# Optimization experiments

Hardware: AMD Instinct MI355X
Metric: run time of the kernel (lower is better)

Reference implementation:

```python
import jax, jax.numpy as jnp
import numpy as np

NUM_EMBEDDINGS = 512
EMBEDDING_DIM = 64
COMMITMENT_COST = 0.25


def setup_inputs() -> dict:
    key = jax.random.key(0)
    k1, k2 = jax.random.split(key)
    x = jax.random.normal(k1, (64, 64, 32, 32), dtype=jnp.float32)  # NCHW, C == embedding_dim
    lim = 1.0 / NUM_EMBEDDINGS
    emb = jax.random.uniform(k2, (NUM_EMBEDDINGS, EMBEDDING_DIM), dtype=jnp.float32,
                             minval=-lim, maxval=lim)
    return {"x": x, "emb": emb}


def reference(x, emb):
    # NCHW -> NHWC
    xp = jnp.transpose(x, (0, 2, 3, 1))  # [B,H,W,D]
    B, H, W, D = xp.shape
    flat = xp.reshape(-1, D)  # [N,D]
    dists = (jnp.sum(flat * flat, axis=1, keepdims=True)
             + jnp.sum(emb * emb, axis=1)
             - 2.0 * jnp.matmul(flat, emb.T))
    idx = jnp.argmin(dists, axis=1)  # [N]
    quantized = emb[idx].reshape(B, H, W, D)
    # losses (note: names follow the original module)
    q_latent_loss = jnp.mean((jax.lax.stop_gradient(quantized) - xp) ** 2)
    e_latent_loss = jnp.mean((quantized - jax.lax.stop_gradient(xp)) ** 2)
    loss = e_latent_loss + COMMITMENT_COST * q_latent_loss
    # straight-through estimator
    quantized = xp + jax.lax.stop_gradient(quantized - xp)
    quantized = jnp.transpose(quantized, (0, 3, 1, 2))  # back to NCHW
    return quantized, loss, idx[:, None]
```

## Files before the change

### kernel.cpp

```cpp
#include <hip/hip_runtime.h>
#include <float.h>

#pragma clang fp contract(off)

#define K_EMB   512
#define D_EMB   64
#define Q_ELEMS 4194304
#define NBLK    1024
#define W_SCR   0.5f
#define XROW    65
#define LCAP    1024

typedef _Float16 f16x8 __attribute__((ext_vector_type(8)));
typedef float    f32x4 __attribute__((ext_vector_type(4)));

__device__ __forceinline__ float np_sumsq64(const float* v) {
    float r[8];
    #pragma unroll
    for (int j = 0; j < 8; ++j) r[j] = v[j] * v[j];
    #pragma unroll
    for (int i = 8; i < 64; i += 8) {
        #pragma unroll
        for (int j = 0; j < 8; ++j) {
            float s = v[i + j] * v[i + j];
            r[j] = r[j] + s;
        }
    }
    return ((r[0] + r[1]) + (r[2] + r[3])) + ((r[4] + r[5]) + (r[6] + r[7]));
}

__global__ __launch_bounds__(256) void vq_prep(const float* __restrict__ emb,
                                               float* __restrict__ t2,
                                               float* __restrict__ t2s512,
                                               f16x8* __restrict__ embA) {
    const int g = blockIdx.x * 256 + threadIdx.x;
    if (g < K_EMB) {
        const float* ep = emb + (g << 6);
        float s = np_sumsq64(ep);
        t2[g]     = s;
        t2s512[g] = 512.0f * s;
    }
    if (g < 4096) {
        const int t = g >> 7;
        const int s = (g >> 6) & 1;
        const int l = g & 63;
        const int code  = t * 16 + (l & 15);
        const int dbase = s * 32 + ((l >> 4) << 3);
        const float* ep = emb + (code << 6) + dbase;
        f16x8 a;
        #pragma unroll
        for (int i = 0; i < 8; ++i) a[i] = (_Float16)(512.0f * ep[i]);
        embA[g] = a;
    }
}

__global__ __launch_bounds__(256) void vq_main(const float* __restrict__ x,
                                               const float* __restrict__ emb,
                                               const float* __restrict__ t2,
                                               const float* __restrict__ t2s512,
                                               const f16x8* __restrict__ embA,
                                               float* __restrict__ out_q,
                                               float* __restrict__ out_idx,
                                               float* __restrict__ partial) {
    const int tid  = threadIdx.x;
    const int lane = tid & 63;
    const int wave = tid >> 6;

    __shared__ float xf[64 * XROW];
    __shared__ float t1s[64];
    __shared__ unsigned long long keys[64];
    __shared__ int   list[LCAP];
    __shared__ int   lcnt;
    __shared__ float red[4];

    {
        const int p = tid & 63;
        const int q = tid >> 6;
        const int np_ = blockIdx.x * 64 + p;
        const float* __restrict__ xs = x + (np_ >> 10) * 65536 + (np_ & 1023);
        #pragma unroll
        for (int j = 0; j < 16; ++j) {
            const int d = q * 16 + j;
            xf[p * XROW + d] = xs[d * 1024];
        }
        if (tid < 64) keys[tid] = 0xFFFFFFFFFFFFFFFFull;
        if (tid == 0) lcnt = 0;
    }
    __syncthreads();

    if (wave == 0) t1s[lane] = np_sumsq64(&xf[lane * XROW]);

    const int bp = 16 * wave + (lane & 15);
    const int bg = lane >> 4;
    f16x8 b0, b1;
    #pragma unroll
    for (int i = 0; i < 8; ++i) {
        b0[i] = (_Float16)xf[bp * XROW + 0 * 32 + bg * 8 + i];
        b1[i] = (_Float16)xf[bp * XROW + 1 * 32 + bg * 8 + i];
    }

    const f32x4 czero = {0.f, 0.f, 0.f, 0.f};
    const float4* __restrict__ t2s4 = (const float4*)t2s512;

    float m = FLT_MAX;
    for (int t = 0; t < 32; ++t) {
        f16x8 a0 = embA[(t * 2 + 0) * 64 + lane];
        f16x8 a1 = embA[(t * 2 + 1) * 64 + lane];
        f32x4 c = __builtin_amdgcn_mfma_f32_16x16x32_f16(a0, b0, czero, 0, 0, 0);
        c = __builtin_amdgcn_mfma_f32_16x16x32_f16(a1, b1, c, 0, 0, 0);
        float4 tv = t2s4[t * 4 + bg];
        float s0 = fmaf(-2.f, c[0], tv.x);
        float s1 = fmaf(-2.f, c[1], tv.y);
        float s2 = fmaf(-2.f, c[2], tv.z);
        float s3 = fmaf(-2.f, c[3], tv.w);
        m = fminf(m, fminf(fminf(s0, s1), fminf(s2, s3)));
    }
    m = fminf(m, __shfl_xor(m, 16));
    m = fminf(m, __shfl_xor(m, 32));
    const float thr = m + W_SCR;

    for (int t = 0; t < 32; ++t) {
        f16x8 a0 = embA[(t * 2 + 0) * 64 + lane];
        f16x8 a1 = embA[(t * 2 + 1) * 64 + lane];
        f32x4 c = __builtin_amdgcn_mfma_f32_16x16x32_f16(a0, b0, czero, 0, 0, 0);
        c = __builtin_amdgcn_mfma_f32_16x16x32_f16(a1, b1, c, 0, 0, 0);
        float4 tv = t2s4[t * 4 + bg];
        #pragma unroll
        for (int j = 0; j < 4; ++j) {
            float sj = fmaf(-2.f, c[j], (j == 0) ? tv.x : (j == 1) ? tv.y
                                       : (j == 2) ? tv.z : tv.w);
            if (sj < thr) {
                const int k = t * 16 + bg * 4 + j;
                int slot = atomicAdd(&lcnt, 1);
                if (slot < LCAP) list[slot] = bp * 512 + k;
            }
        }
    }
    __syncthreads();

    const int ncand = min(lcnt, LCAP);
    for (int i = tid; i < ncand; i += 256) {
        const int v = list[i];
        const int p = v >> 9;
        const int k = v & 511;
        const float* xp = &xf[p * XROW];
        const float* __restrict__ ep = emb + (k << 6);
        float a = 0.f;
        #pragma unroll
        for (int d = 0; d < D_EMB; ++d) a = fmaf(xp[d], ep[d], a);
        float X = t1s[p] + t2[k];
        float dnp = fmaf(-2.f, a, X);
        unsigned long long key =
            ((unsigned long long)__float_as_uint(dnp) << 32) | (unsigned)k;
        atomicMin(&keys[p], key);
    }
    __syncthreads();

    float acc = 0.f;
    {
        const int p = tid & 63;
        const int q = tid >> 6;
        const int n2 = blockIdx.x * 64 + p;
        const int kw = (int)(unsigned)(keys[p] & 0xFFFFFFFFull);
        float* __restrict__ qp = out_q + (n2 >> 10) * 65536 + (n2 & 1023);
        const float4* __restrict__ eq = (const float4*)(emb + (kw << 6) + q * 16);
        #pragma unroll
        for (int j4 = 0; j4 < 4; ++j4) {
            float4 qv = eq[j4];
            const int d = q * 16 + j4 * 4;
            float f0 = qv.x - xf[p * XROW + d + 0];
            float f1 = qv.y - xf[p * XROW + d + 1];
            float f2 = qv.z - xf[p * XROW + d + 2];
            float f3 = qv.w - xf[p * XROW + d + 3];
            acc = fmaf(f0, f0, acc);
            acc = fmaf(f1, f1, acc);
            acc = fmaf(f2, f2, acc);
            acc = fmaf(f3, f3, acc);
            qp[(d + 0) * 1024] = qv.x;
            qp[(d + 1) * 1024] = qv.y;
            qp[(d + 2) * 1024] = qv.z;
            qp[(d + 3) * 1024] = qv.w;
        }
        if (q == 0) out_idx[n2] = (float)kw;
    }

    #pragma unroll
    for (int off = 32; off > 0; off >>= 1) acc += __shfl_down(acc, off);
    if (lane == 0) red[wave] = acc;
    __syncthreads();
    if (tid == 0)
        partial[blockIdx.x] = (red[0] + red[1]) + (red[2] + red[3]);
}

__global__ __launch_bounds__(256) void vq_loss(const float* __restrict__ partial,
                                               float* __restrict__ loss) {
    const int t = threadIdx.x;
    float v = (partial[t] + partial[t + 256]) + (partial[t + 512] + partial[t + 768]);
    #pragma unroll
    for (int off = 32; off > 0; off >>= 1) v += __shfl_down(v, off);
    __shared__ float red[4];
    if ((t & 63) == 0) red[t >> 6] = v;
    __syncthreads();
    if (t == 0)
        loss[0] = 1.25f * ((red[0] + red[1]) + (red[2] + red[3])) / (float)Q_ELEMS;
}

extern "C" void kernel_launch(void* const* d_in, const int* in_sizes, int n_in,
                              void* d_out, int out_size, void* d_ws, size_t ws_size,
                              hipStream_t stream) {
    const float* x   = (const float*)d_in[0];
    const float* emb = (const float*)d_in[1];

    float* out_q    = (float*)d_out;
    float* out_loss = (float*)d_out + Q_ELEMS;
    float* out_idx  = (float*)d_out + Q_ELEMS + 1;

    float* t2      = (float*)d_ws;
    float* t2s512  = t2 + K_EMB;
    float* partial = t2s512 + K_EMB;
    f16x8* embA    = (f16x8*)(partial + 1024);

    vq_prep<<<16, 256, 0, stream>>>(emb, t2, t2s512, embA);
    vq_main<<<NBLK, 256, 0, stream>>>(x, emb, t2, t2s512, embA,
                                      out_q, out_idx, partial);
    vq_loss<<<1, 256, 0, stream>>>(partial, out_loss);
}
```

Baseline: 44.50 us.

## Use single-wave blocks of 16 pixels and cache scores to skip second MFMA pass

The main kernel now runs one 64-thread wave per block covering 16 pixels (4096 blocks), which removes the cross-wave shared reductions and block-wide barriers. Scores from the first MFMA pass are kept in registers as packed half values, so the candidate-filtering pass reuses them instead of reloading the codebook and recomputing the MFMAs. This adds register pressure from the 64-entry half array, and rounding scores to fp16 can shift which codes pass the threshold; fp32 rescoring of candidates still chooses the final index. The loss reduction kernel is widened to sum 4096 partials.

Result: slower. 98.95 us (+122.4%).

```diff
diff --git a/kernel.cpp b/kernel.cpp
--- a/kernel.cpp
+++ b/kernel.cpp
@@ -6,12 +6,14 @@
 #define K_EMB   512
 #define D_EMB   64
 #define Q_ELEMS 4194304
-#define NBLK    1024
+#define PPB     16
+#define NBLK    4096
 #define W_SCR   0.5f
 #define XROW    65
-#define LCAP    1024
+#define LCAP    256
 
 typedef _Float16 f16x8 __attribute__((ext_vector_type(8)));
+typedef _Float16 f16x2 __attribute__((ext_vector_type(2)));
 typedef float    f32x4 __attribute__((ext_vector_type(4)));
 
 __device__ __forceinline__ float np_sumsq64(const float* v) {
@@ -54,55 +56,50 @@
     }
 }
 
-__global__ __launch_bounds__(256) void vq_main(const float* __restrict__ x,
-                                               const float* __restrict__ emb,
-                                               const float* __restrict__ t2,
-                                               const float* __restrict__ t2s512,
-                                               const f16x8* __restrict__ embA,
-                                               float* __restrict__ out_q,
-                                               float* __restrict__ out_idx,
-                                               float* __restrict__ partial) {
-    const int tid  = threadIdx.x;
-    const int lane = tid & 63;
-    const int wave = tid >> 6;
-
-    __shared__ float xf[64 * XROW];
-    __shared__ float t1s[64];
-    __shared__ unsigned long long keys[64];
+__global__ __launch_bounds__(64, 4) void vq_main(const float* __restrict__ x,
+                                                 const float* __restrict__ emb,
+                                                 const float* __restrict__ t2,
+                                                 const float* __restrict__ t2s512,
+                                                 const f16x8* __restrict__ embA,
+                                                 float* __restrict__ out_q,
+                                                 float* __restrict__ out_idx,
+                                                 float* __restrict__ partial) {
+    const int lane = threadIdx.x;
+    const int p16  = lane & 15;
+    const int bg   = lane >> 4;
+
+    __shared__ float xf[PPB * XROW];
+    __shared__ float t1s[PPB];
+    __shared__ unsigned long long keys[PPB];
     __shared__ int   list[LCAP];
     __shared__ int   lcnt;
-    __shared__ float red[4];
-
-    {
-        const int p = tid & 63;
-        const int q = tid >> 6;
-        const int np_ = blockIdx.x * 64 + p;
-        const float* __restrict__ xs = x + (np_ >> 10) * 65536 + (np_ & 1023);
-        #pragma unroll
-        for (int j = 0; j < 16; ++j) {
-            const int d = q * 16 + j;
-            xf[p * XROW + d] = xs[d * 1024];
-        }
-        if (tid < 64) keys[tid] = 0xFFFFFFFFFFFFFFFFull;
-        if (tid == 0) lcnt = 0;
-    }
-    __syncthreads();
-
-    if (wave == 0) t1s[lane] = np_sumsq64(&xf[lane * XROW]);
-
-    const int bp = 16 * wave + (lane & 15);
-    const int bg = lane >> 4;
+
+    const int np_ = blockIdx.x * PPB + p16;
+    const float* __restrict__ xs = x + (np_ >> 10) * 65536 + (np_ & 1023);
+    #pragma unroll
+    for (int j = 0; j < 16; ++j) {
+        const int d = bg * 16 + j;
+        xf[p16 * XROW + d] = xs[d * 1024];
+    }
+    if (lane < PPB) keys[lane] = 0xFFFFFFFFFFFFFFFFull;
+    if (lane == 0) lcnt = 0;
+    __syncthreads();
+
+    if (lane < PPB) t1s[lane] = np_sumsq64(&xf[lane * XROW]);
+
     f16x8 b0, b1;
     #pragma unroll
     for (int i = 0; i < 8; ++i) {
-        b0[i] = (_Float16)xf[bp * XROW + 0 * 32 + bg * 8 + i];
-        b1[i] = (_Float16)xf[bp * XROW + 1 * 32 + bg * 8 + i];
+        b0[i] = (_Float16)xf[p16 * XROW + 0 * 32 + bg * 8 + i];
+        b1[i] = (_Float16)xf[p16 * XROW + 1 * 32 + bg * 8 + i];
     }
 
     const f32x4 czero = {0.f, 0.f, 0.f, 0.f};
     const float4* __restrict__ t2s4 = (const float4*)t2s512;
 
+    f16x2 hv[64];
     float m = FLT_MAX;
+    #pragma unroll
     for (int t = 0; t < 32; ++t) {
         f16x8 a0 = embA[(t * 2 + 0) * 64 + lane];
         f16x8 a1 = embA[(t * 2 + 1) * 64 + lane];
@@ -113,33 +110,35 @@
         float s1 = fmaf(-2.f, c[1], tv.y);
         float s2 = fmaf(-2.f, c[2], tv.z);
         float s3 = fmaf(-2.f, c[3], tv.w);
+        f16x2 p01, p23;
+        p01[0] = (_Float16)s0; p01[1] = (_Float16)s1;
+        p23[0] = (_Float16)s2; p23[1] = (_Float16)s3;
+        hv[t * 2 + 0] = p01;
+        hv[t * 2 + 1] = p23;
         m = fminf(m, fminf(fminf(s0, s1), fminf(s2, s3)));
     }
     m = fminf(m, __shfl_xor(m, 16));
     m = fminf(m, __shfl_xor(m, 32));
     const float thr = m + W_SCR;
 
+    #pragma unroll
     for (int t = 0; t < 32; ++t) {
-        f16x8 a0 = embA[(t * 2 + 0) * 64 + lane];
-        f16x8 a1 = embA[(t * 2 + 1) * 64 + lane];
-        f32x4 c = __builtin_amdgcn_mfma_f32_16x16x32_f16(a0, b0, czero, 0, 0, 0);
-        c = __builtin_amdgcn_mfma_f32_16x16x32_f16(a1, b1, c, 0, 0, 0);
-        float4 tv = t2s4[t * 4 + bg];
-        #pragma unroll
-        for (int j = 0; j < 4; ++j) {
-            float sj = fmaf(-2.f, c[j], (j == 0) ? tv.x : (j == 1) ? tv.y
-                                       : (j == 2) ? tv.z : tv.w);
-            if (sj < thr) {
-                const int k = t * 16 + bg * 4 + j;
-                int slot = atomicAdd(&lcnt, 1);
-                if (slot < LCAP) list[slot] = bp * 512 + k;
-            }
-        }
+        f16x2 p01 = hv[t * 2 + 0];
+        f16x2 p23 = hv[t * 2 + 1];
+        float s0 = (float)p01[0];
+        float s1 = (float)p01[1];
+        float s2 = (float)p23[0];
+        float s3 = (float)p23[1];
+        const int kb = t * 16 + bg * 4;
+        if (s0 < thr) { int s = atomicAdd(&lcnt, 1); if (s < LCAP) list[s] = p16 * 512 + kb + 0; }
+        if (s1 < thr) { int s = atomicAdd(&lcnt, 1); if (s < LCAP) list[s] = p16 * 512 + kb + 1; }
+        if (s2 < thr) { int s = atomicAdd(&lcnt, 1); if (s < LCAP) list[s] = p16 * 512 + kb + 2; }
+        if (s3 < thr) { int s = atomicAdd(&lcnt, 1); if (s < LCAP) list[s] = p16 * 512 + kb + 3; }
     }
     __syncthreads();
 
     const int ncand = min(lcnt, LCAP);
-    for (int i = tid; i < ncand; i += 256) {
+    for (int i = lane; i < ncand; i += 64) {
         const int v = list[i];
         const int p = v >> 9;
         const int k = v & 511;
@@ -158,20 +157,17 @@
 
     float acc = 0.f;
     {
-        const int p = tid & 63;
-        const int q = tid >> 6;
-        const int n2 = blockIdx.x * 64 + p;
-        const int kw = (int)(unsigned)(keys[p] & 0xFFFFFFFFull);
-        float* __restrict__ qp = out_q + (n2 >> 10) * 65536 + (n2 & 1023);
-        const float4* __restrict__ eq = (const float4*)(emb + (kw << 6) + q * 16);
+        const int kw = (int)(unsigned)(keys[p16] & 0xFFFFFFFFull);
+        float* __restrict__ qp = out_q + (np_ >> 10) * 65536 + (np_ & 1023);
+        const float4* __restrict__ eq = (const float4*)(emb + (kw << 6) + bg * 16);
         #pragma unroll
         for (int j4 = 0; j4 < 4; ++j4) {
             float4 qv = eq[j4];
-            const int d = q * 16 + j4 * 4;
-            float f0 = qv.x - xf[p * XROW + d + 0];
-            float f1 = qv.y - xf[p * XROW + d + 1];
-            float f2 = qv.z - xf[p * XROW + d + 2];
-            float f3 = qv.w - xf[p * XROW + d + 3];
+            const int d = bg * 16 + j4 * 4;
+            float f0 = qv.x - xf[p16 * XROW + d + 0];
+            float f1 = qv.y - xf[p16 * XROW + d + 1];
+            float f2 = qv.z - xf[p16 * XROW + d + 2];
+            float f3 = qv.w - xf[p16 * XROW + d + 3];
             acc = fmaf(f0, f0, acc);
             acc = fmaf(f1, f1, acc);
             acc = fmaf(f2, f2, acc);
@@ -181,21 +177,24 @@
             qp[(d + 2) * 1024] = qv.z;
             qp[(d + 3) * 1024] = qv.w;
         }
-        if (q == 0) out_idx[n2] = (float)kw;
+        if (bg == 0) out_idx[np_] = (float)kw;
     }
 
     #pragma unroll
     for (int off = 32; off > 0; off >>= 1) acc += __shfl_down(acc, off);
-    if (lane == 0) red[wave] = acc;
-    __syncthreads();
-    if (tid == 0)
-        partial[blockIdx.x] = (red[0] + red[1]) + (red[2] + red[3]);
+    if (lane == 0) partial[blockIdx.x] = acc;
 }
 
 __global__ __launch_bounds__(256) void vq_loss(const float* __restrict__ partial,
                                                float* __restrict__ loss) {
     const int t = threadIdx.x;
-    float v = (partial[t] + partial[t + 256]) + (partial[t + 512] + partial[t + 768]);
+    float v = 0.f;
+    #pragma unroll
+    for (int i = 0; i < 16; i += 2) {
+        float a = partial[t + (i + 0) * 256];
+        float b = partial[t + (i + 1) * 256];
+        v = v + (a + b);
+    }
     #pragma unroll
     for (int off = 32; off > 0; off >>= 1) v += __shfl_down(v, off);
     __shared__ float red[4];
@@ -218,10 +217,10 @@
     float* t2      = (float*)d_ws;
     float* t2s512  = t2 + K_EMB;
     float* partial = t2s512 + K_EMB;
-    f16x8* embA    = (f16x8*)(partial + 1024);
+    f16x8* embA    = (f16x8*)(partial + 4096);
 
     vq_prep<<<16, 256, 0, stream>>>(emb, t2, t2s512, embA);
-    vq_main<<<NBLK, 256, 0, stream>>>(x, emb, t2, t2s512, embA,
-                                      out_q, out_idx, partial);
+    vq_main<<<NBLK, 64, 0, stream>>>(x, emb, t2, t2s512, embA,
+                                     out_q, out_idx, partial);
     vq_loss<<<1, 256, 0, stream>>>(partial, out_loss);
 }
```
